# Kernel tuning notes

Hardware: AMD Instinct MI355X
Metric: run time of the kernel (lower is better)

The kernel has to match this reference:

```python
import jax, jax.numpy as jnp
import numpy as np

N = 50000
E = 1600000
D_IN = 512
EPS = 1e-5


def setup_inputs() -> dict:
    key = jax.random.key(0)
    ks = jax.random.split(key, 20)
    p = lambda k, shape: jax.random.normal(k, shape, dtype=jnp.float32) * 0.05
    return {
        "x": jax.random.normal(ks[0], (N, D_IN), dtype=jnp.float32),
        "edge_index": jax.random.randint(ks[1], (2, E), 0, N),
        "edge_weight": jax.random.uniform(ks[2], (E,), dtype=jnp.float32),
        # conv1: ChebConv(512->400) with K=1,2,3 (weight per Chebyshev order)
        "W1a": p(ks[3], (1, D_IN, 400)), "b1a": p(ks[4], (400,)),
        "W1b": p(ks[5], (2, D_IN, 400)), "b1b": p(ks[6], (400,)),
        "W1c": p(ks[7], (3, D_IN, 400)), "b1c": p(ks[8], (400,)),
        "g1": jnp.ones((1200,), jnp.float32), "beta1": jnp.zeros((1200,), jnp.float32),
        # conv2: ChebConv(1200->100) with K=1,2,3
        "W2a": p(ks[9], (1, 1200, 100)), "b2a": p(ks[10], (100,)),
        "W2b": p(ks[11], (2, 1200, 100)), "b2b": p(ks[12], (100,)),
        "W2c": p(ks[13], (3, 1200, 100)), "b2c": p(ks[14], (100,)),
        "g2": jnp.ones((300,), jnp.float32), "beta2": jnp.zeros((300,), jnp.float32),
        "Wl": p(ks[15], (300, 10)), "bl": p(ks[16], (10,)),
    }


def _cheb(x, row, col, norm, W, b):
    """PyG ChebConv forward: out = sum_k T_k(L_hat) x @ W[k] + b.
    L_hat (sym norm, lambda_max=2) = -D^{-1/2} A D^{-1/2}, zero diagonal,
    applied as scatter: (L_hat h)[col] += norm_e * h[row]."""
    K = W.shape[0]
    n = x.shape[0]
    prop = lambda h: jax.ops.segment_sum(norm[:, None] * h[row], col, num_segments=n)
    out = x @ W[0]
    Tx_prev, Tx = x, None
    if K >= 2:
        Tx = prop(x)
        out = out + Tx @ W[1]
    for k in range(2, K):
        Tx_new = 2.0 * prop(Tx) - Tx_prev
        out = out + Tx_new @ W[k]
        Tx_prev, Tx = Tx, Tx_new
    return out + b


def _bn(h, g, beta):
    # BatchNorm over nodes (training-mode batch statistics, biased var)
    mu = h.mean(axis=0)
    var = h.var(axis=0)
    return (h - mu) * jax.lax.rsqrt(var + EPS) * g + beta


def reference(x, edge_index, edge_weight, W1a, b1a, W1b, b1b, W1c, b1c, g1, beta1,
              W2a, b2a, W2b, b2b, W2c, b2c, g2, beta2, Wl, bl):
    row, col = edge_index[0], edge_index[1]
    deg = jax.ops.segment_sum(edge_weight, row, num_segments=x.shape[0])
    safe = jnp.where(deg > 0, deg, 1.0)
    dis = jnp.where(deg > 0, jax.lax.rsqrt(safe), 0.0)  # deg^{-1/2}, inf -> 0
    norm = -dis[row] * edge_weight * dis[col]  # scaled-Laplacian edge weights

    h = jnp.concatenate([
        _cheb(x, row, col, norm, W1a, b1a),
        _cheb(x, row, col, norm, W1b, b1b),
        _cheb(x, row, col, norm, W1c, b1c)], axis=1)  # [N, 1200]
    h = jax.nn.relu(_bn(h, g1, beta1))

    h = jnp.concatenate([
        _cheb(h, row, col, norm, W2a, b2a),
        _cheb(h, row, col, norm, W2b, b2b),
        _cheb(h, row, col, norm, W2c, b2c)], axis=1)  # [N, 300]
    h = _bn(h, g2, beta2)

    logits = h @ Wl + bl  # [N, 10]
    return jax.nn.log_softmax(logits, axis=1)
```

## Files before the change

kernel.cpp:

```cpp
#include <hip/hip_runtime.h>
#include <math.h>

#define EPSB 1e-5f

typedef __attribute__((ext_vector_type(8))) short short8;
typedef __attribute__((ext_vector_type(4))) float floatx4;
typedef __attribute__((ext_vector_type(2))) float floatx2;

__device__ inline float bf2f(unsigned short h) {
  union { unsigned int u; float f; } v; v.u = ((unsigned int)h) << 16; return v.f;
}
__device__ inline unsigned short f2bf(float f) {
  union { float f; unsigned int u; } v; v.f = f;
  unsigned int r = v.u + 0x7fffu + ((v.u >> 16) & 1u);
  return (unsigned short)(r >> 16);
}

__device__ __forceinline__ void gl2lds16(const unsigned short* g, unsigned short* l) {
  __builtin_amdgcn_global_load_lds(
      (const __attribute__((address_space(1))) unsigned int*)g,
      (__attribute__((address_space(3))) unsigned int*)l, 16, 0, 0);
}

__device__ __forceinline__ void pk4(floatx2* a, uint4 g, floatx2 wv) {
  unsigned int u[4] = {g.x, g.y, g.z, g.w};
#pragma unroll
  for (int j = 0; j < 4; j++) {
    union { unsigned int q; float f; } lo, hi;
    lo.q = u[j] << 16;
    hi.q = u[j] & 0xffff0000u;
    floatx2 v; v[0] = lo.f; v[1] = hi.f;
    asm("v_pk_fma_f32 %0, %1, %2, %0" : "+v"(a[j]) : "v"(v), "v"(wv));
  }
}


__global__ void degcnt_kernel(const int* __restrict__ row, const int* __restrict__ col,
                              const float* __restrict__ ew,
                              float* __restrict__ deg, int* __restrict__ cnt, int E) {
  int e = blockIdx.x * blockDim.x + threadIdx.x;
  if (e < E) {
    atomicAdd(&deg[row[e]], ew[e]);
    atomicAdd(&cnt[col[e]], 1);
  }
}

__global__ void dis_kernel(float* deg, int n) {
  int i = blockIdx.x * blockDim.x + threadIdx.x;
  if (i < n) { float d = deg[i]; deg[i] = d > 0.f ? rsqrtf(d) : 0.f; }
}

__global__ __launch_bounds__(1024) void scan1_kernel(const int* __restrict__ cnt,
                                                     int* __restrict__ off,
                                                     int* __restrict__ bsum, int n) {
  __shared__ int buf[1024];
  int tid = threadIdx.x;
  int idx = blockIdx.x * 1024 + tid;
  int v = (idx < n) ? cnt[idx] : 0;
  buf[tid] = v;
  __syncthreads();
  for (int s = 1; s < 1024; s <<= 1) {
    int t = (tid >= s) ? buf[tid - s] : 0;
    __syncthreads();
    if (tid >= s) buf[tid] += t;
    __syncthreads();
  }
  if (idx < n) off[idx] = buf[tid] - v;
  if (tid == 1023) bsum[blockIdx.x] = buf[1023];
}

__global__ void scan2_kernel(int* __restrict__ bsum, int* __restrict__ off,
                             int nb, int n) {
  if (threadIdx.x == 0 && blockIdx.x == 0) {
    int run = 0;
    for (int k = 0; k < nb; k++) { int t = bsum[k]; bsum[k] = run; run += t; }
    off[n] = run;
  }
}

__global__ void scan3_kernel(int* __restrict__ off, const int* __restrict__ bsum, int n) {
  int i = blockIdx.x * blockDim.x + threadIdx.x;
  if (i < n) off[i] += bsum[i >> 10];
}

__global__ void copy_kernel(const int* __restrict__ src, int* __restrict__ dst, int n) {
  int i = blockIdx.x * blockDim.x + threadIdx.x;
  if (i < n) dst[i] = src[i];
}

__global__ void fill_kernel(const int* __restrict__ row, const int* __restrict__ col,
                            const float* __restrict__ ew, const float* __restrict__ dis,
                            int* __restrict__ wptr, int2* __restrict__ ePack, int E) {
  int e = blockIdx.x * blockDim.x + threadIdx.x;
  if (e < E) {
    int r = row[e], c = col[e];
    int p = atomicAdd(&wptr[c], 1);
    float nv = -dis[r] * ew[e] * dis[c];
    ePack[p] = make_int2(r, __float_as_int(nv));
  }
}


__global__ void cast_x_kernel(const float* __restrict__ x, unsigned short* __restrict__ xb,
                              int N) {
  int idx = blockIdx.x * blockDim.x + threadIdx.x;
  if (idx >= N * 128) return;
  int row = idx >> 7, c4 = idx & 127;
  float4 v = *reinterpret_cast<const float4*>(x + (size_t)row * 512 + c4 * 4);
  union { unsigned int u[2]; } p;
  p.u[0] = (unsigned int)f2bf(v.x) | ((unsigned int)f2bf(v.y) << 16);
  p.u[1] = (unsigned int)f2bf(v.z) | ((unsigned int)f2bf(v.w) << 16);
  *reinterpret_cast<uint2*>(xb + (size_t)row * 1536 + c4 * 4) = make_uint2(p.u[0], p.u[1]);
}

__global__ void wprep_kernel(const float* __restrict__ W, unsigned short* __restrict__ Bt,
                             int Ktot, int Nout, int ldBt, int rowOff) {
  int idx = blockIdx.x * blockDim.x + threadIdx.x;
  if (idx >= Ktot * Nout) return;
  int k = idx / Nout, n = idx - k * Nout;
  Bt[(size_t)(rowOff + n) * ldBt + k] = f2bf(W[idx]);
}

__global__ void padzero_kernel(unsigned short* __restrict__ h, int N) {
  int i = blockIdx.x * blockDim.x + threadIdx.x;
  if (i >= N * 2) return;
  *reinterpret_cast<uint4*>(h + (size_t)(i >> 1) * 1216 + 1200 + (i & 1) * 8) =
      make_uint4(0, 0, 0, 0);
}

__global__ void bcat_kernel(const float* __restrict__ a, const float* __restrict__ b,
                            const float* __restrict__ c, float* __restrict__ dst) {
  int i = threadIdx.x;
  if (i < 100) dst[i] = a[i];
  else if (i < 200) dst[i] = b[i - 100];
  else if (i < 300) dst[i] = c[i - 200];
}

__global__ __launch_bounds__(256) void prop_chunk_kernel(
    unsigned short* __restrict__ base, int ld,
    int srcCol, int dstCol, int subCol,
    const int* __restrict__ off, const int2* __restrict__ ePack,
    float scale, int N) {
  int chunk = blockIdx.x & 7;
  int g = blockIdx.x >> 3;
  int tid = threadIdx.x;
  int slot = (tid >> 3) & 3;
  int c8 = tid & 7;
  int v = g * 8 + (tid >> 5);
  bool valid = v < N;
  int vv = valid ? v : N - 1;
  int co = chunk * 64 + c8 * 8;
  const unsigned short* src = base + srcCol + co;
  int s = off[vv], e = off[vv + 1];
  int len = e - s;
  int s0 = s + (len * slot >> 2);
  int e0 = s + (len * (slot + 1) >> 2);
  floatx2 a2[4] = {}, b2[4] = {};
  int i = s0;
  for (; i + 3 < e0; i += 4) {
    int2 p0 = ePack[i];
    int2 p1 = ePack[i + 1];
    int2 p2 = ePack[i + 2];
    int2 p3 = ePack[i + 3];
    uint4 g0 = *reinterpret_cast<const uint4*>(src + (size_t)p0.x * ld);
    uint4 g1 = *reinterpret_cast<const uint4*>(src + (size_t)p1.x * ld);
    uint4 g2 = *reinterpret_cast<const uint4*>(src + (size_t)p2.x * ld);
    uint4 g3 = *reinterpret_cast<const uint4*>(src + (size_t)p3.x * ld);
    floatx2 w0; w0[0] = w0[1] = __int_as_float(p0.y);
    floatx2 w1; w1[0] = w1[1] = __int_as_float(p1.y);
    floatx2 w2; w2[0] = w2[1] = __int_as_float(p2.y);
    floatx2 w3; w3[0] = w3[1] = __int_as_float(p3.y);
    pk4(a2, g0, w0);
    pk4(b2, g1, w1);
    pk4(a2, g2, w2);
    pk4(b2, g3, w3);
  }
  for (; i < e0; i++) {
    int2 p = ePack[i];
    uint4 gg = *reinterpret_cast<const uint4*>(src + (size_t)p.x * ld);
    floatx2 wv; wv[0] = wv[1] = __int_as_float(p.y);
    pk4(a2, gg, wv);
  }
  float a[8];
#pragma unroll
  for (int j = 0; j < 4; j++) {
    a[2 * j]     = a2[j][0] + b2[j][0];
    a[2 * j + 1] = a2[j][1] + b2[j][1];
  }
#pragma unroll
  for (int j = 0; j < 8; j++) {
    a[j] += __shfl_xor(a[j], 8);
    a[j] += __shfl_xor(a[j], 16);
  }
  if (slot != 0 || !valid) return;
  if (subCol >= 0) {
    uint4 sv = *reinterpret_cast<const uint4*>(base + subCol + co + (size_t)v * ld);
    a[0] = scale * a[0] - bf2f((unsigned short)(sv.x & 0xffff));
    a[1] = scale * a[1] - bf2f((unsigned short)(sv.x >> 16));
    a[2] = scale * a[2] - bf2f((unsigned short)(sv.y & 0xffff));
    a[3] = scale * a[3] - bf2f((unsigned short)(sv.y >> 16));
    a[4] = scale * a[4] - bf2f((unsigned short)(sv.z & 0xffff));
    a[5] = scale * a[5] - bf2f((unsigned short)(sv.z >> 16));
    a[6] = scale * a[6] - bf2f((unsigned short)(sv.w & 0xffff));
    a[7] = scale * a[7] - bf2f((unsigned short)(sv.w >> 16));
  }
  uint4 o;
  o.x = (unsigned int)f2bf(a[0]) | ((unsigned int)f2bf(a[1]) << 16);
  o.y = (unsigned int)f2bf(a[2]) | ((unsigned int)f2bf(a[3]) << 16);
  o.z = (unsigned int)f2bf(a[4]) | ((unsigned int)f2bf(a[5]) << 16);
  o.w = (unsigned int)f2bf(a[6]) | ((unsigned int)f2bf(a[7]) << 16);
  *reinterpret_cast<uint4*>(base + dstCol + co + (size_t)v * ld) = o;
}

__global__ void prop_z_kernel(const unsigned short* __restrict__ Zcat,
                              const int* __restrict__ off, const int2* __restrict__ ePack,
                              float* __restrict__ h2f, unsigned short* __restrict__ U1) {
  int v = blockIdx.x;
  int f8 = threadIdx.x;
  if (f8 >= 38) return;
  int s = off[v], e = off[v + 1];
  floatx2 a2[4] = {}, b2[4] = {};
  int i = s;
  for (; i + 3 < e; i += 4) {
    int2 p0 = ePack[i];
    int2 p1 = ePack[i + 1];
    int2 p2 = ePack[i + 2];
    int2 p3 = ePack[i + 3];
    uint4 g0 = *reinterpret_cast<const uint4*>(Zcat + (size_t)p0.x * 304 + f8 * 8);
    uint4 g1 = *reinterpret_cast<const uint4*>(Zcat + (size_t)p1.x * 304 + f8 * 8);
    uint4 g2 = *reinterpret_cast<const uint4*>(Zcat + (size_t)p2.x * 304 + f8 * 8);
    uint4 g3 = *reinterpret_cast<const uint4*>(Zcat + (size_t)p3.x * 304 + f8 * 8);
    floatx2 w0; w0[0] = w0[1] = __int_as_float(p0.y);
    floatx2 w1; w1[0] = w1[1] = __int_as_float(p1.y);
    floatx2 w2; w2[0] = w2[1] = __int_as_float(p2.y);
    floatx2 w3; w3[0] = w3[1] = __int_as_float(p3.y);
    pk4(a2, g0, w0);
    pk4(b2, g1, w1);
    pk4(a2, g2, w2);
    pk4(b2, g3, w3);
  }
  for (; i < e; i++) {
    int2 p = ePack[i];
    uint4 raw = *reinterpret_cast<const uint4*>(Zcat + (size_t)p.x * 304 + f8 * 8);
    floatx2 wv; wv[0] = wv[1] = __int_as_float(p.y);
    pk4(a2, raw, wv);
  }
  float a[8];
#pragma unroll
  for (int j = 0; j < 4; j++) {
    a[2 * j]     = a2[j][0] + b2[j][0];
    a[2 * j + 1] = a2[j][1] + b2[j][1];
  }
  if (f8 < 25) {
    float* p = h2f + (size_t)v * 300 + 100 + f8 * 8;
#pragma unroll
    for (int j = 0; j < 8; j++) p[j] += a[j];
  } else {
    uint4 o;
    o.x = (unsigned int)f2bf(a[0]) | ((unsigned int)f2bf(a[1]) << 16);
    o.y = (unsigned int)f2bf(a[2]) | ((unsigned int)f2bf(a[3]) << 16);
    o.z = (unsigned int)f2bf(a[4]) | ((unsigned int)f2bf(a[5]) << 16);
    o.w = (unsigned int)f2bf(a[6]) | ((unsigned int)f2bf(a[7]) << 16);
    *reinterpret_cast<uint4*>(U1 + (size_t)v * 104 + (f8 - 25) * 8) = o;
  }
}

__global__ void prop_u_kernel(const unsigned short* __restrict__ U1,
                              const int* __restrict__ off, const int2* __restrict__ ePack,
                              const unsigned short* __restrict__ Zcat,
                              float* __restrict__ h2f) {
  int v = blockIdx.x;
  int f8 = threadIdx.x;
  if (f8 >= 13) return;
  int s = off[v], e = off[v + 1];
  floatx2 a2[4] = {}, b2[4] = {};
  int i = s;
  for (; i + 3 < e; i += 4) {
    int2 p0 = ePack[i];
    int2 p1 = ePack[i + 1];
    int2 p2 = ePack[i + 2];
    int2 p3 = ePack[i + 3];
    uint4 g0 = *reinterpret_cast<const uint4*>(U1 + (size_t)p0.x * 104 + f8 * 8);
    uint4 g1 = *reinterpret_cast<const uint4*>(U1 + (size_t)p1.x * 104 + f8 * 8);
    uint4 g2 = *reinterpret_cast<const uint4*>(U1 + (size_t)p2.x * 104 + f8 * 8);
    uint4 g3 = *reinterpret_cast<const uint4*>(U1 + (size_t)p3.x * 104 + f8 * 8);
    floatx2 w0; w0[0] = w0[1] = __int_as_float(p0.y);
    floatx2 w1; w1[0] = w1[1] = __int_as_float(p1.y);
    floatx2 w2; w2[0] = w2[1] = __int_as_float(p2.y);
    floatx2 w3; w3[0] = w3[1] = __int_as_float(p3.y);
    pk4(a2, g0, w0);
    pk4(b2, g1, w1);
    pk4(a2, g2, w2);
    pk4(b2, g3, w3);
  }
  for (; i < e; i++) {
    int2 p = ePack[i];
    uint4 raw = *reinterpret_cast<const uint4*>(U1 + (size_t)p.x * 104 + f8 * 8);
    floatx2 wv; wv[0] = wv[1] = __int_as_float(p.y);
    pk4(a2, raw, wv);
  }
  float a[8];
#pragma unroll
  for (int j = 0; j < 4; j++) {
    a[2 * j]     = a2[j][0] + b2[j][0];
    a[2 * j + 1] = a2[j][1] + b2[j][1];
  }
  const unsigned short* z2 = Zcat + (size_t)v * 304 + 200;
  float* p = h2f + (size_t)v * 300 + 200;
#pragma unroll
  for (int j = 0; j < 8; j++) {
    int c = f8 * 8 + j;
    if (c < 100) p[c] += 2.f * a[j] - bf2f(z2[c]);
  }
}

__global__ __launch_bounds__(256) void gemm_bf16_kernel(
    const unsigned short* __restrict__ A, int lda,
    const unsigned short* __restrict__ Bt, int ldb,
    int M, int Nc, int K,
    const float* __restrict__ bias,
    unsigned short* __restrict__ Cb, float* __restrict__ Cf, int ldc, int c0,
    int accumulate) {
  __shared__ __align__(16) unsigned short As[128 * 32];
  __shared__ __align__(16) unsigned short Bs[128 * 32];
  int colTiles = (Nc + 127) >> 7;
  int rowTiles = (M + 127) >> 7;
  int L = blockIdx.x;
  int xcd = L & 7, slot = L >> 3;
  int rpx = (rowTiles + 7) >> 3;
  int rloc = slot / colTiles;
  int ct = slot - rloc * colTiles;
  int rt = xcd * rpx + rloc;
  if (rt >= rowTiles) return;
  int row0 = rt << 7, col0 = ct << 7;

  int tid = threadIdx.x;
  int wave = tid >> 6, lane = tid & 63;
  int q = lane >> 4, mn = lane & 15;
  int wr = wave >> 1, wc = wave & 1;
  floatx4 acc[4][4] = {};

  const unsigned short* ga[2];
  const unsigned short* gb[2];
  unsigned short* la[2];
  unsigned short* lb[2];
#pragma unroll
  for (int j = 0; j < 2; j++) {
    int c = j * 256 + tid;
    int r = c >> 2, cw = (c & 3) * 8;
    int gr = row0 + r; if (gr > M - 1) gr = M - 1;
    ga[j] = A + (size_t)gr * lda + cw;
    int gn = col0 + r; if (gn > Nc - 1) gn = Nc - 1;
    gb[j] = Bt + (size_t)gn * ldb + cw;
    la[j] = &As[(j * 256 + wave * 64) * 8];
    lb[j] = &Bs[(j * 256 + wave * 64) * 8];
  }

  for (int k0 = 0; k0 < K; k0 += 32) {
#pragma unroll
    for (int j = 0; j < 2; j++) {
      gl2lds16(ga[j] + k0, la[j]);
      gl2lds16(gb[j] + k0, lb[j]);
    }
    __syncthreads();

    short8 af[4], bf[4];
#pragma unroll
    for (int i = 0; i < 4; i++) {
      af[i] = *reinterpret_cast<const short8*>(&As[(wr * 64 + i * 16 + mn) * 32 + q * 8]);
      bf[i] = *reinterpret_cast<const short8*>(&Bs[(wc * 64 + i * 16 + mn) * 32 + q * 8]);
    }
#pragma unroll
    for (int mi = 0; mi < 4; mi++)
#pragma unroll
      for (int ni = 0; ni < 4; ni++)
        acc[mi][ni] = __builtin_amdgcn_mfma_f32_16x16x32_bf16(af[mi], bf[ni], acc[mi][ni], 0, 0, 0);
    __syncthreads();
  }

#pragma unroll
  for (int mi = 0; mi < 4; mi++) {
#pragma unroll
    for (int ni = 0; ni < 4; ni++) {
      int gcol = col0 + wc * 64 + ni * 16 + mn;
      if (gcol >= Nc) continue;
      float b = bias ? bias[gcol] : 0.f;
#pragma unroll
      for (int r = 0; r < 4; r++) {
        int grow = row0 + wr * 64 + mi * 16 + q * 4 + r;
        if (grow >= M) continue;
        float v = acc[mi][ni][r] + b;
        if (Cb) {
          Cb[(size_t)grow * ldc + c0 + gcol] = f2bf(v);
        } else {
          float* p = Cf + (size_t)grow * ldc + c0 + gcol;
          if (accumulate) v += *p;
          *p = v;
        }
      }
    }
  }
}

__global__ void bn_stats_bf16_kernel(const unsigned short* __restrict__ h, int ld, int C,
                                     int N, float* __restrict__ sums) {
  int c = blockIdx.x * blockDim.x + threadIdx.x;
  if (c >= C) return;
  int r0 = blockIdx.y * 256;
  int r1 = min(N, r0 + 256);
  float s = 0.f, s2 = 0.f;
  for (int r = r0; r < r1; r++) {
    float v = bf2f(h[(size_t)r * ld + c]);
    s += v; s2 += v * v;
  }
  atomicAdd(&sums[c], s);
  atomicAdd(&sums[C + c], s2);
}

__global__ void scsh_kernel(const float* __restrict__ sums, const float* __restrict__ g,
                            const float* __restrict__ beta, float invN, int C,
                            float* __restrict__ scSh) {
  int c = blockIdx.x * blockDim.x + threadIdx.x;
  if (c >= C) return;
  float mu = sums[c] * invN;
  float var = sums[C + c] * invN - mu * mu;
  float s = rsqrtf(var + EPSB) * g[c];
  scSh[c] = s;
  scSh[C + c] = beta[c] - mu * s;
}

__global__ void bn_apply_bf16_kernel(unsigned short* __restrict__ h, int ld, int C8, int N,
                                     const float* __restrict__ scSh, int Cfull, int relu) {
  int idx = blockIdx.x * blockDim.x + threadIdx.x;
  if (idx >= N * C8) return;
  int row = idx / C8, c8 = idx - row * C8;
  unsigned short* p = h + (size_t)row * ld + c8 * 8;
  uint4 raw = *reinterpret_cast<uint4*>(p);
  float v[8];
  v[0] = bf2f((unsigned short)(raw.x & 0xffff)); v[1] = bf2f((unsigned short)(raw.x >> 16));
  v[2] = bf2f((unsigned short)(raw.y & 0xffff)); v[3] = bf2f((unsigned short)(raw.y >> 16));
  v[4] = bf2f((unsigned short)(raw.z & 0xffff)); v[5] = bf2f((unsigned short)(raw.z >> 16));
  v[6] = bf2f((unsigned short)(raw.w & 0xffff)); v[7] = bf2f((unsigned short)(raw.w >> 16));
#pragma unroll
  for (int j = 0; j < 8; j++) {
    int c = c8 * 8 + j;
    float o = v[j] * scSh[c] + scSh[Cfull + c];
    if (relu) o = fmaxf(o, 0.f);
    v[j] = o;
  }
  uint4 o;
  o.x = (unsigned int)f2bf(v[0]) | ((unsigned int)f2bf(v[1]) << 16);
  o.y = (unsigned int)f2bf(v[2]) | ((unsigned int)f2bf(v[3]) << 16);
  o.z = (unsigned int)f2bf(v[4]) | ((unsigned int)f2bf(v[5]) << 16);
  o.w = (unsigned int)f2bf(v[6]) | ((unsigned int)f2bf(v[7]) << 16);
  *reinterpret_cast<uint4*>(p) = o;
}

__global__ void bn_stats_kernel(const float* __restrict__ h, int C, int N,
                                float* __restrict__ sums) {
  int c = blockIdx.x * blockDim.x + threadIdx.x;
  if (c >= C) return;
  int r0 = blockIdx.y * 256;
  int r1 = min(N, r0 + 256);
  float s = 0.f, s2 = 0.f;
  for (int r = r0; r < r1; r++) {
    float v = h[(size_t)r * C + c];
    s += v; s2 += v * v;
  }
  atomicAdd(&sums[c], s);
  atomicAdd(&sums[C + c], s2);
}

__global__ void bn_apply_kernel(float* __restrict__ h, int C, int N,
                                const float* __restrict__ sums, const float* __restrict__ g,
                                const float* __restrict__ beta, float invN, int relu) {
  int C4 = C >> 2;
  int c4 = blockIdx.x * blockDim.x + threadIdx.x;
  if (c4 >= C4) return;
  float sc[4], sh[4];
#pragma unroll
  for (int j = 0; j < 4; j++) {
    int c = c4 * 4 + j;
    float mu = sums[c] * invN;
    float var = sums[C + c] * invN - mu * mu;
    float s = rsqrtf(var + EPSB) * g[c];
    sc[j] = s; sh[j] = beta[c] - mu * s;
  }
  int r0 = blockIdx.y * 256, r1 = min(N, r0 + 256);
  for (int r = r0; r < r1; r++) {
    float4* p = reinterpret_cast<float4*>(h + (size_t)r * C) + c4;
    float4 v = *p;
    v.x = v.x * sc[0] + sh[0]; v.y = v.y * sc[1] + sh[1];
    v.z = v.z * sc[2] + sh[2]; v.w = v.w * sc[3] + sh[3];
    if (relu) {
      v.x = fmaxf(v.x, 0.f); v.y = fmaxf(v.y, 0.f);
      v.z = fmaxf(v.z, 0.f); v.w = fmaxf(v.w, 0.f);
    }
    *p = v;
  }
}


__global__ __launch_bounds__(256) void final_bn_kernel(const float* __restrict__ h2,
                                                       const float* __restrict__ scSh,
                                                       const float* __restrict__ Wl,
                                                       const float* __restrict__ bl,
                                                       float* __restrict__ out, int N) {
  __shared__ float Ws[3000];
  __shared__ float S[600];
  for (int i = threadIdx.x; i < 3000; i += 256) Ws[i] = Wl[i];
  for (int i = threadIdx.x; i < 600; i += 256) S[i] = scSh[i];
  __syncthreads();
  int r = blockIdx.x * blockDim.x + threadIdx.x;
  if (r >= N) return;
  float acc[10];
#pragma unroll
  for (int c = 0; c < 10; c++) acc[c] = bl[c];
  const float* hr = h2 + (size_t)r * 300;
  for (int k = 0; k < 300; k++) {
    float x = hr[k] * S[k] + S[300 + k];
#pragma unroll
    for (int c = 0; c < 10; c++) acc[c] += x * Ws[k * 10 + c];
  }
  float mx = acc[0];
#pragma unroll
  for (int c = 1; c < 10; c++) mx = fmaxf(mx, acc[c]);
  float se = 0.f;
#pragma unroll
  for (int c = 0; c < 10; c++) se += expf(acc[c] - mx);
  float lz = mx + logf(se);
#pragma unroll
  for (int c = 0; c < 10; c++) out[(size_t)r * 10 + c] = acc[c] - lz;
}

__global__ __launch_bounds__(256) void final_kernel(const float* __restrict__ h2,
                                                    const float* __restrict__ Wl,
                                                    const float* __restrict__ bl,
                                                    float* __restrict__ out, int N) {
  __shared__ float Ws[3000];
  for (int i = threadIdx.x; i < 3000; i += 256) Ws[i] = Wl[i];
  __syncthreads();
  int r = blockIdx.x * blockDim.x + threadIdx.x;
  if (r >= N) return;
  float acc[10];
#pragma unroll
  for (int c = 0; c < 10; c++) acc[c] = bl[c];
  const float* hr = h2 + (size_t)r * 300;
  for (int k = 0; k < 300; k++) {
    float x = hr[k];
#pragma unroll
    for (int c = 0; c < 10; c++) acc[c] += x * Ws[k * 10 + c];
  }
  float mx = acc[0];
#pragma unroll
  for (int c = 1; c < 10; c++) mx = fmaxf(mx, acc[c]);
  float se = 0.f;
#pragma unroll
  for (int c = 0; c < 10; c++) se += expf(acc[c] - mx);
  float lz = mx + logf(se);
#pragma unroll
  for (int c = 0; c < 10; c++) out[(size_t)r * 10 + c] = acc[c] - lz;
}


__global__ void prop_kernel(const float* __restrict__ src, int srcLd4, int D4,
                            const int* __restrict__ off, const int2* __restrict__ ePack,
                            float* __restrict__ dst, int dstLd4,
                            const float* __restrict__ sub, int subLd4, float scale) {
  int v = blockIdx.x;
  int f4 = threadIdx.x;
  if (f4 >= D4) return;
  int s = off[v], e = off[v + 1];
  float ax = 0.f, ay = 0.f, az = 0.f, aw = 0.f;
  for (int i = s; i < e; i++) {
    int2 p = ePack[i];
    float w = __int_as_float(p.y);
    const float4 hv = *reinterpret_cast<const float4*>(src + ((size_t)p.x * srcLd4 + f4) * 4);
    ax += w * hv.x; ay += w * hv.y; az += w * hv.z; aw += w * hv.w;
  }
  float4 o;
  if (sub) {
    const float4 sv = *reinterpret_cast<const float4*>(sub + ((size_t)v * subLd4 + f4) * 4);
    o.x = scale * ax - sv.x; o.y = scale * ay - sv.y;
    o.z = scale * az - sv.z; o.w = scale * aw - sv.w;
  } else {
    o.x = ax; o.y = ay; o.z = az; o.w = aw;
  }
  *reinterpret_cast<float4*>(dst + ((size_t)v * dstLd4 + f4) * 4) = o;
}

#define BM 64
#define BN 64
#define BK 16

__global__ __launch_bounds__(256) void gemm_kernel(
    const float* __restrict__ A, int lda,
    const float* __restrict__ B, int ldb,
    float* __restrict__ C, int ldc, int c0,
    int M, int Nc, int K,
    const float* __restrict__ bias, int accumulate) {
  __shared__ float As[BK][BM + 4];
  __shared__ float Bs[BK][BN + 4];
  int tid = threadIdx.x;
  int tx = tid & 15, ty = tid >> 4;
  int row0 = blockIdx.y * BM, col0 = blockIdx.x * BN;
  float acc[4][4] = {};
  int aM = tid >> 2;
  int aK = (tid & 3) << 2;
  int bK = tid >> 4;
  int bN = (tid & 15) << 2;
  for (int k0 = 0; k0 < K; k0 += BK) {
    float4 av = make_float4(0.f, 0.f, 0.f, 0.f);
    int ar = row0 + aM;
    if (ar < M && k0 + aK < K)
      av = *reinterpret_cast<const float4*>(A + (size_t)ar * lda + k0 + aK);
    As[aK + 0][aM] = av.x; As[aK + 1][aM] = av.y;
    As[aK + 2][aM] = av.z; As[aK + 3][aM] = av.w;
    float4 bv = make_float4(0.f, 0.f, 0.f, 0.f);
    int bc = col0 + bN;
    if (bc < Nc && k0 + bK < K)
      bv = *reinterpret_cast<const float4*>(B + (size_t)(k0 + bK) * ldb + bc);
    Bs[bK][bN + 0] = bv.x; Bs[bK][bN + 1] = bv.y;
    Bs[bK][bN + 2] = bv.z; Bs[bK][bN + 3] = bv.w;
    __syncthreads();
#pragma unroll
    for (int k = 0; k < BK; k++) {
      float a0 = As[k][ty * 4 + 0], a1 = As[k][ty * 4 + 1];
      float a2 = As[k][ty * 4 + 2], a3 = As[k][ty * 4 + 3];
      float b0 = Bs[k][tx * 4 + 0], b1 = Bs[k][tx * 4 + 1];
      float b2 = Bs[k][tx * 4 + 2], b3 = Bs[k][tx * 4 + 3];
      acc[0][0] += a0 * b0; acc[0][1] += a0 * b1; acc[0][2] += a0 * b2; acc[0][3] += a0 * b3;
      acc[1][0] += a1 * b0; acc[1][1] += a1 * b1; acc[1][2] += a1 * b2; acc[1][3] += a1 * b3;
      acc[2][0] += a2 * b0; acc[2][1] += a2 * b1; acc[2][2] += a2 * b2; acc[2][3] += a2 * b3;
      acc[3][0] += a3 * b0; acc[3][1] += a3 * b1; acc[3][2] += a3 * b2; acc[3][3] += a3 * b3;
    }
    __syncthreads();
  }
#pragma unroll
  for (int i = 0; i < 4; i++) {
    int r = row0 + ty * 4 + i;
    if (r >= M) continue;
#pragma unroll
    for (int j = 0; j < 4; j++) {
      int c = col0 + tx * 4 + j;
      if (c >= Nc) continue;
      float v = acc[i][j];
      if (bias) v += bias[c];
      float* p = C + (size_t)r * ldc + c0 + c;
      if (accumulate) *p += v; else *p = v;
    }
  }
}


static inline int gemm_grid(int M, int Nc) {
  int rowTiles = (M + 127) >> 7;
  int colTiles = (Nc + 127) >> 7;
  int rpx = (rowTiles + 7) >> 3;
  return 8 * rpx * colTiles;
}

extern "C" void kernel_launch(void* const* d_in, const int* in_sizes, int n_in,
                              void* d_out, int out_size, void* d_ws, size_t ws_size,
                              hipStream_t stream) {
  const float* x   = (const float*)d_in[0];
  const int*   ei  = (const int*)d_in[1];
  const float* ew  = (const float*)d_in[2];
  const float* W1a = (const float*)d_in[3];
  const float* b1a = (const float*)d_in[4];
  const float* W1b = (const float*)d_in[5];
  const float* b1b = (const float*)d_in[6];
  const float* W1c = (const float*)d_in[7];
  const float* b1c = (const float*)d_in[8];
  const float* g1  = (const float*)d_in[9];
  const float* be1 = (const float*)d_in[10];
  const float* W2a = (const float*)d_in[11];
  const float* b2a = (const float*)d_in[12];
  const float* W2b = (const float*)d_in[13];
  const float* b2b = (const float*)d_in[14];
  const float* W2c = (const float*)d_in[15];
  const float* b2c = (const float*)d_in[16];
  const float* g2  = (const float*)d_in[17];
  const float* be2 = (const float*)d_in[18];
  const float* Wl  = (const float*)d_in[19];
  const float* bl  = (const float*)d_in[20];
  float* out = (float*)d_out;

  const int N = in_sizes[0] / 512;
  const int E = in_sizes[1] / 2;
  const int* row = ei;
  const int* col = ei + E;
  (void)n_in; (void)out_size;

  int eb = (E + 255) / 256;
  int nb = (N + 255) / 256;
  int nb1 = (N + 1023) / 1024;

  char* ws = (char*)d_ws;
  size_t o = 0;
  int2*  ePack = (int2*)(ws + o);  o += (size_t)E * 8;
  float* dis   = (float*)(ws + o); o += (size_t)N * 4;
  int*   cnt   = (int*)(ws + o);   o += (size_t)N * 4;
  int*   off   = (int*)(ws + o);   o += (size_t)(N + 4) * 4;
  int*   wptr  = (int*)(ws + o);   o += (size_t)N * 4;
  int*   bsum  = (int*)(ws + o);   o += (size_t)(nb1 + 4) * 4;
  float* sums  = (float*)(ws + o); o += 2400 * 4;
  float* scSh  = (float*)(ws + o); o += 2400 * 4;
  float* bcat  = (float*)(ws + o); o += 304 * 4;
  o = (o + 255) & ~(size_t)255;
  size_t oCommon = o;

  size_t oA = oCommon;
  unsigned short* Bt1a = (unsigned short*)(ws + oA); oA += (size_t)400 * 512 * 2;
  unsigned short* Bt1b = (unsigned short*)(ws + oA); oA += (size_t)400 * 1024 * 2;
  unsigned short* Bt1c = (unsigned short*)(ws + oA); oA += (size_t)400 * 1536 * 2;
  unsigned short* Bt2cat0 = (unsigned short*)(ws + oA); oA += (size_t)304 * 1216 * 2;
  unsigned short* Bt2z    = (unsigned short*)(ws + oA); oA += (size_t)304 * 1216 * 2;
  oA = (oA + 255) & ~(size_t)255;
  unsigned short* h1n = (unsigned short*)(ws + oA); oA += (size_t)N * 1216 * 2;
  oA = (oA + 255) & ~(size_t)255;
  float* h2f = (float*)(ws + oA); oA += (size_t)N * 300 * 4;
  oA = (oA + 255) & ~(size_t)255;
  unsigned short* Xcat = (unsigned short*)(ws + oA); oA += (size_t)N * 1536 * 2;
  unsigned short* Zcat = Xcat;
  unsigned short* U1 = Xcat + (size_t)N * 304;

  bool planA = (ws_size >= oA);

  hipMemsetAsync(dis, 0, (size_t)N * 4, stream);
  hipMemsetAsync(cnt, 0, (size_t)N * 4, stream);
  degcnt_kernel<<<eb, 256, 0, stream>>>(row, col, ew, dis, cnt, E);
  dis_kernel<<<nb, 256, 0, stream>>>(dis, N);
  scan1_kernel<<<nb1, 1024, 0, stream>>>(cnt, off, bsum, N);
  scan2_kernel<<<1, 64, 0, stream>>>(bsum, off, nb1, N);
  scan3_kernel<<<nb, 256, 0, stream>>>(off, bsum, N);
  copy_kernel<<<nb, 256, 0, stream>>>(off, wptr, N);
  fill_kernel<<<eb, 256, 0, stream>>>(row, col, ew, dis, wptr, ePack, E);

  if (planA) {
    wprep_kernel<<<(400 * 512 + 255) / 256, 256, 0, stream>>>(W1a, Bt1a, 512, 400, 512, 0);
    wprep_kernel<<<(400 * 1024 + 255) / 256, 256, 0, stream>>>(W1b, Bt1b, 1024, 400, 1024, 0);
    wprep_kernel<<<(400 * 1536 + 255) / 256, 256, 0, stream>>>(W1c, Bt1c, 1536, 400, 1536, 0);
    hipMemsetAsync(Bt2cat0, 0, (size_t)304 * 1216 * 2, stream);
    hipMemsetAsync(Bt2z, 0, (size_t)304 * 1216 * 2, stream);
    wprep_kernel<<<(100 * 1200 + 255) / 256, 256, 0, stream>>>(W2a, Bt2cat0, 1200, 100, 1216, 0);
    wprep_kernel<<<(100 * 1200 + 255) / 256, 256, 0, stream>>>(W2b, Bt2cat0, 1200, 100, 1216, 100);
    wprep_kernel<<<(100 * 1200 + 255) / 256, 256, 0, stream>>>(W2c, Bt2cat0, 1200, 100, 1216, 200);
    wprep_kernel<<<(100 * 1200 + 255) / 256, 256, 0, stream>>>(W2b + 1200 * 100, Bt2z, 1200, 100, 1216, 0);
    wprep_kernel<<<(100 * 1200 + 255) / 256, 256, 0, stream>>>(W2c + 1200 * 100, Bt2z, 1200, 100, 1216, 100);
    wprep_kernel<<<(100 * 1200 + 255) / 256, 256, 0, stream>>>(W2c + 2 * 1200 * 100, Bt2z, 1200, 100, 1216, 200);
    bcat_kernel<<<1, 320, 0, stream>>>(b2a, b2b, b2c, bcat);
    cast_x_kernel<<<(N * 128 + 255) / 256, 256, 0, stream>>>(x, Xcat, N);
    padzero_kernel<<<(N * 2 + 255) / 256, 256, 0, stream>>>(h1n, N);

    int gridP = ((N + 7) / 8) * 8;
    prop_chunk_kernel<<<gridP, 256, 0, stream>>>(Xcat, 1536, 0, 512, -1,
                                                 off, ePack, 1.f, N);
    prop_chunk_kernel<<<gridP, 256, 0, stream>>>(Xcat, 1536, 512, 1024, 0,
                                                 off, ePack, 2.f, N);

    int gA = gemm_grid(N, 400);
    gemm_bf16_kernel<<<gA, 256, 0, stream>>>(Xcat, 1536, Bt1a, 512, N, 400, 512,
                                             b1a, h1n, nullptr, 1216, 0, 0);
    gemm_bf16_kernel<<<gA, 256, 0, stream>>>(Xcat, 1536, Bt1b, 1024, N, 400, 1024,
                                             b1b, h1n, nullptr, 1216, 400, 0);
    gemm_bf16_kernel<<<gA, 256, 0, stream>>>(Xcat, 1536, Bt1c, 1536, N, 400, 1536,
                                             b1c, h1n, nullptr, 1216, 800, 0);

    hipMemsetAsync(sums, 0, 2400 * 4, stream);
    dim3 s1g((1200 + 255) / 256, (N + 255) / 256);
    bn_stats_bf16_kernel<<<s1g, 256, 0, stream>>>(h1n, 1216, 1200, N, sums);
    scsh_kernel<<<(1200 + 255) / 256, 256, 0, stream>>>(sums, g1, be1, 1.f / (float)N, 1200, scSh);
    bn_apply_bf16_kernel<<<((size_t)N * 150 + 255) / 256, 256, 0, stream>>>(
        h1n, 1216, 150, N, scSh, 1200, 1);

    int gB0 = gemm_grid(N, 300);
    gemm_bf16_kernel<<<gB0, 256, 0, stream>>>(h1n, 1216, Bt2cat0, 1216, N, 300, 1216,
                                              bcat, nullptr, h2f, 300, 0, 0);

    int gBz = gemm_grid(N, 304);
    gemm_bf16_kernel<<<gBz, 256, 0, stream>>>(h1n, 1216, Bt2z, 1216, N, 304, 1216,
                                              nullptr, Zcat, nullptr, 304, 0, 0);

    prop_z_kernel<<<N, 64, 0, stream>>>(Zcat, off, ePack, h2f, U1);
    prop_u_kernel<<<N, 64, 0, stream>>>(U1, off, ePack, Zcat, h2f);

    hipMemsetAsync(sums, 0, 2400 * 4, stream);
    dim3 s2g((300 + 255) / 256, (N + 255) / 256);
    bn_stats_kernel<<<s2g, 256, 0, stream>>>(h2f, 300, N, sums);
    scsh_kernel<<<(300 + 255) / 256, 256, 0, stream>>>(sums, g2, be2, 1.f / (float)N, 300, scSh);
    final_bn_kernel<<<nb, 256, 0, stream>>>(h2f, scSh, Wl, bl, out, N);
    return;
  }

  size_t oB = oCommon;
  float* h2 = (float*)(ws + oB); oB += (size_t)N * 300 * 4;
  oB = (oB + 255) & ~(size_t)255;
  float* h1 = (float*)(ws + oB); oB += (size_t)N * 1200 * 4;
  oB = (oB + 255) & ~(size_t)255;
  size_t avail = (ws_size > oB) ? (ws_size - oB) : 0;
  int C1 = 64;
  { const int opts[4] = {512, 256, 128, 64};
    for (int i = 0; i < 4; i++)
      if ((size_t)2 * N * opts[i] * 4 <= avail) { C1 = opts[i]; break; } }
  int C2 = 100;
  { const int opts[6] = {1200, 600, 400, 300, 200, 100};
    for (int i = 0; i < 6; i++)
      if ((size_t)2 * N * opts[i] * 4 <= avail) { C2 = opts[i]; break; } }
  int maxC = C1 > C2 ? C1 : C2;
  float* S1 = (float*)(ws + oB);
  float* S2 = S1 + (size_t)N * maxC;

  dim3 g1d((400 + BN - 1) / BN, (N + BM - 1) / BM);
  gemm_kernel<<<g1d, 256, 0, stream>>>(x, 512, W1a, 400, h1, 1200, 0,   N, 400, 512, b1a, 0);
  gemm_kernel<<<g1d, 256, 0, stream>>>(x, 512, W1b, 400, h1, 1200, 400, N, 400, 512, b1b, 0);
  gemm_kernel<<<g1d, 256, 0, stream>>>(x, 512, W1c, 400, h1, 1200, 800, N, 400, 512, b1c, 0);
  for (int c = 0; c < 512; c += C1) {
    int D4 = C1 / 4;
    int bt = ((D4 + 63) / 64) * 64;
    prop_kernel<<<N, bt, 0, stream>>>(x + c, 128, D4, off, ePack, S1, D4, nullptr, 0, 1.f);
    gemm_kernel<<<g1d, 256, 0, stream>>>(S1, C1, W1b + (size_t)(512 + c) * 400, 400, h1, 1200, 400, N, 400, C1, nullptr, 1);
    gemm_kernel<<<g1d, 256, 0, stream>>>(S1, C1, W1c + (size_t)(512 + c) * 400, 400, h1, 1200, 800, N, 400, C1, nullptr, 1);
    prop_kernel<<<N, bt, 0, stream>>>(S1, D4, D4, off, ePack, S2, D4, x + c, 128, 2.f);
    gemm_kernel<<<g1d, 256, 0, stream>>>(S2, C1, W1c + (size_t)(2 * 512 + c) * 400, 400, h1, 1200, 800, N, 400, C1, nullptr, 1);
  }

  hipMemsetAsync(sums, 0, 2400 * 4, stream);
  dim3 s1g((1200 + 255) / 256, (N + 255) / 256);
  bn_stats_kernel<<<s1g, 256, 0, stream>>>(h1, 1200, N, sums);
  dim3 a1g((300 + 63) / 64, (N + 255) / 256);
  bn_apply_kernel<<<a1g, 64, 0, stream>>>(h1, 1200, N, sums, g1, be1, 1.f / (float)N, 1);

  dim3 g2d((100 + BN - 1) / BN, (N + BM - 1) / BM);
  gemm_kernel<<<g2d, 256, 0, stream>>>(h1, 1200, W2a, 100, h2, 300, 0,   N, 100, 1200, b2a, 0);
  gemm_kernel<<<g2d, 256, 0, stream>>>(h1, 1200, W2b, 100, h2, 300, 100, N, 100, 1200, b2b, 0);
  gemm_kernel<<<g2d, 256, 0, stream>>>(h1, 1200, W2c, 100, h2, 300, 200, N, 100, 1200, b2c, 0);
  for (int c = 0; c < 1200; c += C2) {
    int D4 = C2 / 4;
    int bt = ((D4 + 63) / 64) * 64;
    prop_kernel<<<N, bt, 0, stream>>>(h1 + c, 300, D4, off, ePack, S1, D4, nullptr, 0, 1.f);
    gemm_kernel<<<g2d, 256, 0, stream>>>(S1, C2, W2b + (size_t)(1200 + c) * 100, 100, h2, 300, 100, N, 100, C2, nullptr, 1);
    gemm_kernel<<<g2d, 256, 0, stream>>>(S1, C2, W2c + (size_t)(1200 + c) * 100, 100, h2, 300, 200, N, 100, C2, nullptr, 1);
    prop_kernel<<<N, bt, 0, stream>>>(S1, D4, D4, off, ePack, S2, D4, h1 + c, 300, 2.f);
    gemm_kernel<<<g2d, 256, 0, stream>>>(S2, C2, W2c + (size_t)(2 * 1200 + c) * 100, 100, h2, 300, 200, N, 100, C2, nullptr, 1);
  }

  hipMemsetAsync(sums, 0, 2400 * 4, stream);
  dim3 s2g((300 + 255) / 256, (N + 255) / 256);
  bn_stats_kernel<<<s2g, 256, 0, stream>>>(h2, 300, N, sums);
  dim3 a2g((75 + 63) / 64, (N + 255) / 256);
  bn_apply_kernel<<<a2g, 64, 0, stream>>>(h2, 300, N, sums, g2, be2, 1.f / (float)N, 0);

  final_kernel<<<nb, 256, 0, stream>>>(h2, Wl, bl, out, N);
}
```

Baseline: 1.791 ms.

## Fuse per-branch Chebyshev GEMMs into single launches with per-tile K truncation

The three layer-1 GEMMs become one 1200-column GEMM over a packed, zero-padded weight matrix. Each column tile stops its K loop at the Chebyshev order its columns need. The two layer-2 GEMMs become one 608-column GEMM with a dual epilogue: biased fp32 output for the first 300 columns and bf16 Z output for columns 304 and up. This cuts wasted padded-column compute and launch count, and lets the shared A rows be reused across more column tiles. In exchange, tiles with different K lengths share one grid, which can leave the work unevenly balanced across blocks.

```diff
diff --git a/kernel.cpp b/kernel.cpp
--- a/kernel.cpp
+++ b/kernel.cpp
@@ -129,11 +129,14 @@
 }
 
 __global__ void bcat_kernel(const float* __restrict__ a, const float* __restrict__ b,
-                            const float* __restrict__ c, float* __restrict__ dst) {
-  int i = threadIdx.x;
-  if (i < 100) dst[i] = a[i];
-  else if (i < 200) dst[i] = b[i - 100];
-  else if (i < 300) dst[i] = c[i - 200];
+                            const float* __restrict__ c, float* __restrict__ dst, int seg) {
+  int i = blockIdx.x * blockDim.x + threadIdx.x;
+  if (i >= 3 * seg) return;
+  float v;
+  if (i < seg) v = a[i];
+  else if (i < 2 * seg) v = b[i - seg];
+  else v = c[i - 2 * seg];
+  dst[i] = v;
 }
 
 __global__ __launch_bounds__(256) void prop_chunk_kernel(
@@ -320,7 +323,7 @@
     int M, int Nc, int K,
     const float* __restrict__ bias,
     unsigned short* __restrict__ Cb, float* __restrict__ Cf, int ldc, int c0,
-    int accumulate) {
+    int accumulate, int l1mode, int dual) {
   __shared__ __align__(16) unsigned short As[128 * 32];
   __shared__ __align__(16) unsigned short Bs[128 * 32];
   int colTiles = (Nc + 127) >> 7;
@@ -334,6 +337,9 @@
   if (rt >= rowTiles) return;
   int row0 = rt << 7, col0 = ct << 7;
 
+  int Kt = K;
+  if (l1mode) Kt = (col0 + 127 < 400) ? 512 : ((col0 + 127 < 800) ? 1024 : K);
+
   int tid = threadIdx.x;
   int wave = tid >> 6, lane = tid & 63;
   int q = lane >> 4, mn = lane & 15;
@@ -356,7 +362,7 @@
     lb[j] = &Bs[(j * 256 + wave * 64) * 8];
   }
 
-  for (int k0 = 0; k0 < K; k0 += 32) {
+  for (int k0 = 0; k0 < Kt; k0 += 32) {
 #pragma unroll
     for (int j = 0; j < 2; j++) {
       gl2lds16(ga[j] + k0, la[j]);
@@ -384,18 +390,37 @@
     for (int ni = 0; ni < 4; ni++) {
       int gcol = col0 + wc * 64 + ni * 16 + mn;
       if (gcol >= Nc) continue;
-      float b = bias ? bias[gcol] : 0.f;
-#pragma unroll
-      for (int r = 0; r < 4; r++) {
-        int grow = row0 + wr * 64 + mi * 16 + q * 4 + r;
-        if (grow >= M) continue;
-        float v = acc[mi][ni][r] + b;
-        if (Cb) {
-          Cb[(size_t)grow * ldc + c0 + gcol] = f2bf(v);
-        } else {
-          float* p = Cf + (size_t)grow * ldc + c0 + gcol;
-          if (accumulate) v += *p;
-          *p = v;
+      if (dual) {
+        if (gcol < 300) {
+          float b = bias[gcol];
+#pragma unroll
+          for (int r = 0; r < 4; r++) {
+            int grow = row0 + wr * 64 + mi * 16 + q * 4 + r;
+            if (grow >= M) continue;
+            Cf[(size_t)grow * 300 + gcol] = acc[mi][ni][r] + b;
+          }
+        } else if (gcol >= 304) {
+#pragma unroll
+          for (int r = 0; r < 4; r++) {
+            int grow = row0 + wr * 64 + mi * 16 + q * 4 + r;
+            if (grow >= M) continue;
+            Cb[(size_t)grow * 304 + (gcol - 304)] = f2bf(acc[mi][ni][r]);
+          }
+        }
+      } else {
+        float b = bias ? bias[gcol] : 0.f;
+#pragma unroll
+        for (int r = 0; r < 4; r++) {
+          int grow = row0 + wr * 64 + mi * 16 + q * 4 + r;
+          if (grow >= M) continue;
+          float v = acc[mi][ni][r] + b;
+          if (Cb) {
+            Cb[(size_t)grow * ldc + c0 + gcol] = f2bf(v);
+          } else {
+            float* p = Cf + (size_t)grow * ldc + c0 + gcol;
+            if (accumulate) v += *p;
+            *p = v;
+          }
         }
       }
     }
@@ -706,16 +731,14 @@
   int*   bsum  = (int*)(ws + o);   o += (size_t)(nb1 + 4) * 4;
   float* sums  = (float*)(ws + o); o += 2400 * 4;
   float* scSh  = (float*)(ws + o); o += 2400 * 4;
-  float* bcat  = (float*)(ws + o); o += 304 * 4;
+  float* bcat1 = (float*)(ws + o); o += 1200 * 4;
+  float* bcat2 = (float*)(ws + o); o += 304 * 4;
   o = (o + 255) & ~(size_t)255;
   size_t oCommon = o;
 
   size_t oA = oCommon;
-  unsigned short* Bt1a = (unsigned short*)(ws + oA); oA += (size_t)400 * 512 * 2;
-  unsigned short* Bt1b = (unsigned short*)(ws + oA); oA += (size_t)400 * 1024 * 2;
-  unsigned short* Bt1c = (unsigned short*)(ws + oA); oA += (size_t)400 * 1536 * 2;
-  unsigned short* Bt2cat0 = (unsigned short*)(ws + oA); oA += (size_t)304 * 1216 * 2;
-  unsigned short* Bt2z    = (unsigned short*)(ws + oA); oA += (size_t)304 * 1216 * 2;
+  unsigned short* BtL1 = (unsigned short*)(ws + oA); oA += (size_t)1280 * 1536 * 2;
+  unsigned short* BtL2 = (unsigned short*)(ws + oA); oA += (size_t)640 * 1216 * 2;
   oA = (oA + 255) & ~(size_t)255;
   unsigned short* h1n = (unsigned short*)(ws + oA); oA += (size_t)N * 1216 * 2;
   oA = (oA + 255) & ~(size_t)255;
@@ -738,18 +761,19 @@
   fill_kernel<<<eb, 256, 0, stream>>>(row, col, ew, dis, wptr, ePack, E);
 
   if (planA) {
-    wprep_kernel<<<(400 * 512 + 255) / 256, 256, 0, stream>>>(W1a, Bt1a, 512, 400, 512, 0);
-    wprep_kernel<<<(400 * 1024 + 255) / 256, 256, 0, stream>>>(W1b, Bt1b, 1024, 400, 1024, 0);
-    wprep_kernel<<<(400 * 1536 + 255) / 256, 256, 0, stream>>>(W1c, Bt1c, 1536, 400, 1536, 0);
-    hipMemsetAsync(Bt2cat0, 0, (size_t)304 * 1216 * 2, stream);
-    hipMemsetAsync(Bt2z, 0, (size_t)304 * 1216 * 2, stream);
-    wprep_kernel<<<(100 * 1200 + 255) / 256, 256, 0, stream>>>(W2a, Bt2cat0, 1200, 100, 1216, 0);
-    wprep_kernel<<<(100 * 1200 + 255) / 256, 256, 0, stream>>>(W2b, Bt2cat0, 1200, 100, 1216, 100);
-    wprep_kernel<<<(100 * 1200 + 255) / 256, 256, 0, stream>>>(W2c, Bt2cat0, 1200, 100, 1216, 200);
-    wprep_kernel<<<(100 * 1200 + 255) / 256, 256, 0, stream>>>(W2b + 1200 * 100, Bt2z, 1200, 100, 1216, 0);
-    wprep_kernel<<<(100 * 1200 + 255) / 256, 256, 0, stream>>>(W2c + 1200 * 100, Bt2z, 1200, 100, 1216, 100);
-    wprep_kernel<<<(100 * 1200 + 255) / 256, 256, 0, stream>>>(W2c + 2 * 1200 * 100, Bt2z, 1200, 100, 1216, 200);
-    bcat_kernel<<<1, 320, 0, stream>>>(b2a, b2b, b2c, bcat);
+    hipMemsetAsync(BtL1, 0, (size_t)1280 * 1536 * 2, stream);
+    hipMemsetAsync(BtL2, 0, (size_t)640 * 1216 * 2, stream);
+    wprep_kernel<<<(400 * 512 + 255) / 256, 256, 0, stream>>>(W1a, BtL1, 512, 400, 1536, 0);
+    wprep_kernel<<<(400 * 1024 + 255) / 256, 256, 0, stream>>>(W1b, BtL1, 1024, 400, 1536, 400);
+    wprep_kernel<<<(400 * 1536 + 255) / 256, 256, 0, stream>>>(W1c, BtL1, 1536, 400, 1536, 800);
+    wprep_kernel<<<(100 * 1200 + 255) / 256, 256, 0, stream>>>(W2a, BtL2, 1200, 100, 1216, 0);
+    wprep_kernel<<<(100 * 1200 + 255) / 256, 256, 0, stream>>>(W2b, BtL2, 1200, 100, 1216, 100);
+    wprep_kernel<<<(100 * 1200 + 255) / 256, 256, 0, stream>>>(W2c, BtL2, 1200, 100, 1216, 200);
+    wprep_kernel<<<(100 * 1200 + 255) / 256, 256, 0, stream>>>(W2b + 1200 * 100, BtL2, 1200, 100, 1216, 304);
+    wprep_kernel<<<(100 * 1200 + 255) / 256, 256, 0, stream>>>(W2c + 1200 * 100, BtL2, 1200, 100, 1216, 404);
+    wprep_kernel<<<(100 * 1200 + 255) / 256, 256, 0, stream>>>(W2c + 2 * 1200 * 100, BtL2, 1200, 100, 1216, 504);
+    bcat_kernel<<<(1200 + 255) / 256, 256, 0, stream>>>(b1a, b1b, b1c, bcat1, 400);
+    bcat_kernel<<<(300 + 255) / 256, 256, 0, stream>>>(b2a, b2b, b2c, bcat2, 100);
     cast_x_kernel<<<(N * 128 + 255) / 256, 256, 0, stream>>>(x, Xcat, N);
     padzero_kernel<<<(N * 2 + 255) / 256, 256, 0, stream>>>(h1n, N);
 
@@ -759,13 +783,9 @@
     prop_chunk_kernel<<<gridP, 256, 0, stream>>>(Xcat, 1536, 512, 1024, 0,
                                                  off, ePack, 2.f, N);
 
-    int gA = gemm_grid(N, 400);
-    gemm_bf16_kernel<<<gA, 256, 0, stream>>>(Xcat, 1536, Bt1a, 512, N, 400, 512,
-                                             b1a, h1n, nullptr, 1216, 0, 0);
-    gemm_bf16_kernel<<<gA, 256, 0, stream>>>(Xcat, 1536, Bt1b, 1024, N, 400, 1024,
-                                             b1b, h1n, nullptr, 1216, 400, 0);
-    gemm_bf16_kernel<<<gA, 256, 0, stream>>>(Xcat, 1536, Bt1c, 1536, N, 400, 1536,
-                                             b1c, h1n, nullptr, 1216, 800, 0);
+    int gA = gemm_grid(N, 1200);
+    gemm_bf16_kernel<<<gA, 256, 0, stream>>>(Xcat, 1536, BtL1, 1536, N, 1200, 1536,
+                                             bcat1, h1n, nullptr, 1216, 0, 0, 1, 0);
 
     hipMemsetAsync(sums, 0, 2400 * 4, stream);
     dim3 s1g((1200 + 255) / 256, (N + 255) / 256);
@@ -774,13 +794,9 @@
     bn_apply_bf16_kernel<<<((size_t)N * 150 + 255) / 256, 256, 0, stream>>>(
         h1n, 1216, 150, N, scSh, 1200, 1);
 
-    int gB0 = gemm_grid(N, 300);
-    gemm_bf16_kernel<<<gB0, 256, 0, stream>>>(h1n, 1216, Bt2cat0, 1216, N, 300, 1216,
-                                              bcat, nullptr, h2f, 300, 0, 0);
-
-    int gBz = gemm_grid(N, 304);
-    gemm_bf16_kernel<<<gBz, 256, 0, stream>>>(h1n, 1216, Bt2z, 1216, N, 304, 1216,
-                                              nullptr, Zcat, nullptr, 304, 0, 0);
+    int gB = gemm_grid(N, 608);
+    gemm_bf16_kernel<<<gB, 256, 0, stream>>>(h1n, 1216, BtL2, 1216, N, 608, 1216,
+                                             bcat2, Zcat, h2f, 0, 0, 0, 0, 1);
 
     prop_z_kernel<<<N, 64, 0, stream>>>(Zcat, off, ePack, h2f, U1);
     prop_u_kernel<<<N, 64, 0, stream>>>(U1, off, ePack, Zcat, h2f);
```

Result: faster. 1.686 ms (-5.9%).
